# Kernel tuning notes

Hardware: AMD Instinct MI355X
Metric: run time of the kernel (lower is better)

Reference implementation:

```python
import jax, jax.numpy as jnp
import numpy as np

N_QUBITS = 10
N_LAYERS = 2
DIM = 2 ** N_QUBITS


def setup_inputs() -> dict:
    key = jax.random.key(0)
    kx, kw = jax.random.split(key)
    x = jax.random.normal(kx, (16384, DIM), dtype=jnp.float32)
    weights = jax.random.normal(kw, (N_LAYERS, N_QUBITS, 3), dtype=jnp.float32)
    return {"x": x, "weights": weights}


def _rot(phi, theta, omega):
    # qml.Rot(phi, theta, omega) = RZ(omega) @ RY(theta) @ RZ(phi)
    c = jnp.cos(theta / 2).astype(jnp.complex64)
    s = jnp.sin(theta / 2).astype(jnp.complex64)
    ep = jnp.exp(0.5j * phi.astype(jnp.complex64))
    eo = jnp.exp(0.5j * omega.astype(jnp.complex64))
    return jnp.stack([
        jnp.stack([jnp.conj(eo) * jnp.conj(ep) * c, -jnp.conj(eo) * ep * s]),
        jnp.stack([eo * jnp.conj(ep) * s, eo * ep * c]),
    ])


def _apply_1q(state, U, w):
    # state: [B, 2, 2, ..., 2]; wire w lives at axis w+1 (wire 0 = most significant)
    state = jnp.moveaxis(state, w + 1, 1)
    state = jnp.einsum('ij,bj...->bi...', U, state)
    return jnp.moveaxis(state, 1, w + 1)


def _cnot(state, c, t):
    state = jnp.moveaxis(state, (c + 1, t + 1), (1, 2))
    state = state.at[:, 1].set(state[:, 1, ::-1])  # flip target where control==1
    return jnp.moveaxis(state, (1, 2), (c + 1, t + 1))


def _pauliz_signs():
    # S[k, i] = +1 if bit i of basis index k is 0 else -1 (wire 0 most significant)
    idx = np.arange(DIM)
    S = np.stack([1.0 - 2.0 * ((idx >> (N_QUBITS - 1 - i)) & 1)
                  for i in range(N_QUBITS)], axis=1)
    return jnp.asarray(S.astype(np.float32))


def reference(x, weights):
    B = x.shape[0]
    x = x.reshape(B, -1)
    # AmplitudeEmbedding(normalize=True)
    amp = x / jnp.linalg.norm(x, axis=1, keepdims=True)
    state = amp.astype(jnp.complex64).reshape((B,) + (2,) * N_QUBITS)
    # StronglyEntanglingLayers: per layer, Rot on every wire then ring of CNOTs
    for l in range(N_LAYERS):
        for q in range(N_QUBITS):
            phi, theta, omega = weights[l, q, 0], weights[l, q, 1], weights[l, q, 2]
            state = _apply_1q(state, _rot(phi, theta, omega), q)
        r = (l % (N_QUBITS - 1)) + 1  # PennyLane default ranges
        for q in range(N_QUBITS):
            state = _cnot(state, q, (q + r) % N_QUBITS)
    probs = (state.real ** 2 + state.imag ** 2).reshape(B, DIM)
    return probs @ _pauliz_signs()  # [B, n_qubits] PauliZ expvals
```

## Files before the change

kernel.cpp:

```cpp
#include <hip/hip_runtime.h>
#include <math.h>

#define NQ 10
#define DIM 1024
#define NL 2

__global__ void precompute_gates(const float* __restrict__ w, float* __restrict__ g) {
    int t = threadIdx.x;
    if (t < NL * NQ) {
        float phi = w[t * 3 + 0], theta = w[t * 3 + 1], omega = w[t * 3 + 2];
        float c  = cosf(0.5f * theta), s = sinf(0.5f * theta);
        float ap = 0.5f * phi, ao = 0.5f * omega;
        float cs = cosf(ap + ao), ss = sinf(ap + ao);
        float cd = cosf(ap - ao), sd = sinf(ap - ao);
        float* o = g + t * 8;
        o[0] =  c * cs;  o[1] = -c * ss;
        o[2] = -s * cd;  o[3] = -s * sd;
        o[4] =  s * cd;  o[5] = -s * sd;
        o[6] =  c * cs;  o[7] =  c * ss;
    }
}

template<int CTRL>
__device__ __forceinline__ float dppmov(float v) {
    return __int_as_float(
        __builtin_amdgcn_mov_dpp(__float_as_int(v), CTRL, 0xF, 0xF, true));
}

typedef unsigned u32x2 __attribute__((ext_vector_type(2)));
typedef float f2 __attribute__((ext_vector_type(2)));

template<int LM>
__device__ __forceinline__ void plswap(float& d, float& s) {
#if __has_builtin(__builtin_amdgcn_permlane16_swap) && __has_builtin(__builtin_amdgcn_permlane32_swap)
    u32x2 r;
    if constexpr (LM == 16)
        r = __builtin_amdgcn_permlane16_swap(__float_as_uint(d), __float_as_uint(s), false, false);
    else
        r = __builtin_amdgcn_permlane32_swap(__float_as_uint(d), __float_as_uint(s), false, false);
    d = __uint_as_float(r.x);
    s = __uint_as_float(r.y);
#else
    asm("v_mov_b32 %0, %1" : "=v"(s) : "v"(s));
    if constexpr (LM == 16) asm("v_permlane16_swap_b32 %0, %1" : "+v"(d), "+v"(s));
    else                    asm("v_permlane32_swap_b32 %0, %1" : "+v"(d), "+v"(s));
#endif
}

template<int LM>
__device__ __forceinline__ float xfetch(float v) {
    if constexpr (LM == 1)      return dppmov<0xB1>(v);
    else if constexpr (LM == 2) return dppmov<0x4E>(v);
    else if constexpr (LM == 4)
        return __int_as_float(__builtin_amdgcn_ds_swizzle(__float_as_int(v), 0x101F));
    else                        return dppmov<0x128>(v);
}

template<int LM>
__device__ __forceinline__ f2 xfetch2(f2 v) {
    f2 r; r.x = xfetch<LM>(v.x); r.y = xfetch<LM>(v.y); return r;
}

template<int LM>
__device__ __forceinline__ void plswap2(f2 v, f2& d, f2& s) {
    float dx = v.x, sx = v.x; plswap<LM>(dx, sx);
    float dy = v.y, sy = v.y; plswap<LM>(dy, sy);
    d.x = dx; d.y = dy; s.x = sx; s.y = sy;
}

template<int LM>
__device__ __forceinline__ float bfly_add(float v) {
    if constexpr (LM >= 16) { float d = v, s = v; plswap<LM>(d, s); return d + s; }
    else                    return v + xfetch<LM>(v);
}

__device__ __forceinline__ float bfly_full(float v) {
    v = bfly_add<1>(v); v = bfly_add<2>(v); v = bfly_add<4>(v);
    v = bfly_add<8>(v); v = bfly_add<16>(v); v = bfly_add<32>(v);
    return v;
}

template<int P>
__device__ __forceinline__ void rot2(f2 (&R)[8], f2 (&I)[8],
                                     const float* __restrict__ g, int lane) {
    float u00r = g[0], u00i = g[1], u01r = g[2], u01i = g[3];
    float u10r = g[4], u10i = g[5], u11r = g[6], u11i = g[7];
    if constexpr (P == 0) {
        f2 Kr0 = {u00r, u10r}, Ki0 = {u00i, u10i};
        f2 Kr1 = {u01r, u11r}, Ki1 = {u01i, u11i};
        #pragma unroll
        for (int j = 0; j < 8; ++j) {
            f2 ar = R[j], ai = I[j];
            f2 arx = {ar.x, ar.x}, ary = {ar.y, ar.y};
            f2 aix = {ai.x, ai.x}, aiy = {ai.y, ai.y};
            R[j] = Kr0*arx - Ki0*aix + Kr1*ary - Ki1*aiy;
            I[j] = Kr0*aix + Ki0*arx + Kr1*aiy + Ki1*ary;
        }
    } else if constexpr (P <= 3) {
        constexpr int m2 = 1 << (P - 1);
        #pragma unroll
        for (int j = 0; j < 8; ++j) {
            if (!(j & m2)) {
                const int j2 = j | m2;
                f2 a0 = R[j], a0i = I[j], a1 = R[j2], a1i = I[j2];
                R[j]  = u00r*a0 - u00i*a0i + u01r*a1 - u01i*a1i;
                I[j]  = u00r*a0i + u00i*a0 + u01r*a1i + u01i*a1;
                R[j2] = u10r*a0 - u10i*a0i + u11r*a1 - u11i*a1i;
                I[j2] = u10r*a0i + u10i*a0 + u11r*a1i + u11i*a1;
            }
        }
    } else if constexpr (P <= 7) {
        constexpr int LM = 1 << (P - 4);
        const bool hi = (lane & LM) != 0;
        float Ar = hi ? u11r : u00r, Ai = hi ? u11i : u00i;
        float Br = hi ? u10r : u01r, Bi = hi ? u10i : u01i;
        #pragma unroll
        for (int j = 0; j < 8; ++j) {
            f2 pr = xfetch2<LM>(R[j]), pi = xfetch2<LM>(I[j]);
            f2 mr = R[j], mi = I[j];
            R[j] = Ar*mr - Ai*mi + Br*pr - Bi*pi;
            I[j] = Ar*mi + Ai*mr + Br*pi + Bi*pr;
        }
    } else {
        constexpr int LM = 1 << (P - 4);
        const bool hi = (lane & LM) != 0;
        float Cdr = hi ? u10r : u00r, Cdi = hi ? u10i : u00i;
        float Csr = hi ? u11r : u01r, Csi = hi ? u11i : u01i;
        #pragma unroll
        for (int j = 0; j < 8; ++j) {
            f2 dr, sr, di, si;
            plswap2<LM>(R[j], dr, sr);
            plswap2<LM>(I[j], di, si);
            R[j] = Cdr*dr - Cdi*di + Csr*sr - Csi*si;
            I[j] = Cdr*di + Cdi*dr + Csr*si + Csi*sr;
        }
    }
}

template<int PC, int PT>
__device__ __forceinline__ void cnot2(f2 (&R)[8], f2 (&I)[8], int lane) {
    if constexpr (PC >= 4 && PT >= 4) {
        constexpr int LM = 1 << (PT - 4);
        const bool ctrl = (lane & (1 << (PC - 4))) != 0;
        if constexpr (LM >= 16) {
            const bool t = (lane & LM) != 0;
            const bool sel = (ctrl == t);
            #pragma unroll
            for (int j = 0; j < 8; ++j) {
                f2 d, s;  plswap2<LM>(R[j], d, s);  R[j] = sel ? d : s;
                f2 di, si; plswap2<LM>(I[j], di, si); I[j] = sel ? di : si;
            }
        } else {
            #pragma unroll
            for (int j = 0; j < 8; ++j) {
                f2 pr = xfetch2<LM>(R[j]), pi = xfetch2<LM>(I[j]);
                R[j] = ctrl ? pr : R[j];
                I[j] = ctrl ? pi : I[j];
            }
        }
    } else if constexpr (PC >= 4 && PT >= 1) {
        constexpr int m2 = 1 << (PT - 1);
        const bool ctrl = (lane & (1 << (PC - 4))) != 0;
        #pragma unroll
        for (int j = 0; j < 8; ++j) {
            if (!(j & m2)) {
                const int j2 = j | m2;
                f2 a = R[j], b = R[j2];
                R[j] = ctrl ? b : a;  R[j2] = ctrl ? a : b;
                f2 c = I[j], d = I[j2];
                I[j] = ctrl ? d : c;  I[j2] = ctrl ? c : d;
            }
        }
    } else if constexpr (PC >= 4 && PT == 0) {
        const bool ctrl = (lane & (1 << (PC - 4))) != 0;
        #pragma unroll
        for (int j = 0; j < 8; ++j) {
            f2 a = R[j]; f2 sw; sw.x = a.y; sw.y = a.x; R[j] = ctrl ? sw : a;
            f2 b = I[j]; f2 sx; sx.x = b.y; sx.y = b.x; I[j] = ctrl ? sx : b;
        }
    } else if constexpr (PC >= 1 && PT >= 4) {
        constexpr int LM = 1 << (PT - 4);
        constexpr int cm2 = 1 << (PC - 1);
        if constexpr (LM >= 16) {
            const bool t = (lane & LM) != 0;
            #pragma unroll
            for (int j = 0; j < 8; ++j) {
                if (j & cm2) {
                    f2 d, s;  plswap2<LM>(R[j], d, s);  R[j] = t ? d : s;
                    f2 di, si; plswap2<LM>(I[j], di, si); I[j] = t ? di : si;
                }
            }
        } else {
            #pragma unroll
            for (int j = 0; j < 8; ++j) {
                if (j & cm2) { R[j] = xfetch2<LM>(R[j]); I[j] = xfetch2<LM>(I[j]); }
            }
        }
    } else if constexpr (PC == 0 && PT >= 4) {
        constexpr int LM = 1 << (PT - 4);
        if constexpr (LM >= 16) {
            const bool t = (lane & LM) != 0;
            #pragma unroll
            for (int j = 0; j < 8; ++j) {
                float dy = R[j].y, sy = R[j].y; plswap<LM>(dy, sy); R[j].y = t ? dy : sy;
                float ey = I[j].y, fy = I[j].y; plswap<LM>(ey, fy); I[j].y = t ? ey : fy;
            }
        } else {
            #pragma unroll
            for (int j = 0; j < 8; ++j) {
                R[j].y = xfetch<LM>(R[j].y); I[j].y = xfetch<LM>(I[j].y);
            }
        }
    } else if constexpr (PC >= 1 && PT >= 1) {
        constexpr int cm2 = 1 << (PC - 1), tm2 = 1 << (PT - 1);
        #pragma unroll
        for (int j = 0; j < 8; ++j) {
            if ((j & cm2) && !(j & tm2)) {
                const int j2 = j | tm2;
                f2 t = R[j]; R[j] = R[j2]; R[j2] = t;
                f2 u = I[j]; I[j] = I[j2]; I[j2] = u;
            }
        }
    } else if constexpr (PC >= 1 && PT == 0) {
        constexpr int cm2 = 1 << (PC - 1);
        #pragma unroll
        for (int j = 0; j < 8; ++j) {
            if (j & cm2) {
                f2 a = R[j]; R[j].x = a.y; R[j].y = a.x;
                f2 b = I[j]; I[j].x = b.y; I[j].y = b.x;
            }
        }
    } else {
        constexpr int tm2 = 1 << (PT - 1);
        #pragma unroll
        for (int j = 0; j < 8; ++j) {
            if (!(j & tm2)) {
                const int j2 = j | tm2;
                float t = R[j].y; R[j].y = R[j2].y; R[j2].y = t;
                float u = I[j].y; I[j].y = I[j2].y; I[j2].y = u;
            }
        }
    }
}

__global__ __launch_bounds__(256) void qsim(const float* __restrict__ x,
                                            const float* __restrict__ gates,
                                            float* __restrict__ out, int B) {
    const int lane = threadIdx.x & 63;
    const int wave = threadIdx.x >> 6;
    const int row  = blockIdx.x * 4 + wave;
    if (row >= B) return;

    const float* xr = x + (size_t)row * DIM + lane * 16;
    f2 R[8], I[8];
    {
        float4 v0 = *(const float4*)(xr + 0);
        float4 v1 = *(const float4*)(xr + 4);
        float4 v2 = *(const float4*)(xr + 8);
        float4 v3 = *(const float4*)(xr + 12);
        R[0].x=v0.x; R[0].y=v0.y;  R[1].x=v0.z; R[1].y=v0.w;
        R[2].x=v1.x; R[2].y=v1.y;  R[3].x=v1.z; R[3].y=v1.w;
        R[4].x=v2.x; R[4].y=v2.y;  R[5].x=v2.z; R[5].y=v2.w;
        R[6].x=v3.x; R[6].y=v3.y;  R[7].x=v3.z; R[7].y=v3.w;
    }
    f2 n2 = R[0]*R[0];
    #pragma unroll
    for (int j = 1; j < 8; ++j) n2 += R[j]*R[j];
    float nrm = bfly_full(n2.x + n2.y);
    float inv = rsqrtf(nrm);

    {
        const float* g = gates;
        const bool hi = (lane & 32) != 0;
        float Cdr = (hi ? g[4] : g[0]) * inv, Cdi = (hi ? g[5] : g[1]) * inv;
        float Csr = (hi ? g[6] : g[2]) * inv, Csi = (hi ? g[7] : g[3]) * inv;
        #pragma unroll
        for (int j = 0; j < 8; ++j) {
            f2 d, s; plswap2<32>(R[j], d, s);
            R[j] = Cdr*d + Csr*s;
            I[j] = Cdi*d + Csi*s;
        }
    }

    #define ROT(l, q) rot2<9 - (q)>(R, I, gates + ((l) * 10 + (q)) * 8, lane)

    ROT(0,1); ROT(0,2); ROT(0,3); ROT(0,4);
    ROT(0,5); ROT(0,6); ROT(0,7); ROT(0,8); ROT(0,9);
    cnot2<9,8>(R,I,lane); cnot2<8,7>(R,I,lane);
    cnot2<7,6>(R,I,lane); cnot2<6,5>(R,I,lane);
    cnot2<5,4>(R,I,lane); cnot2<4,3>(R,I,lane);
    cnot2<3,2>(R,I,lane); cnot2<2,1>(R,I,lane);
    cnot2<1,0>(R,I,lane); cnot2<0,9>(R,I,lane);

    ROT(1,0); ROT(1,1); ROT(1,2); ROT(1,3); ROT(1,4);
    ROT(1,5); ROT(1,6); ROT(1,7); ROT(1,8); ROT(1,9);
    cnot2<9,7>(R,I,lane); cnot2<8,6>(R,I,lane);
    cnot2<7,5>(R,I,lane); cnot2<6,4>(R,I,lane);
    cnot2<5,3>(R,I,lane); cnot2<4,2>(R,I,lane);
    cnot2<3,1>(R,I,lane); cnot2<2,0>(R,I,lane);
    cnot2<1,9>(R,I,lane); cnot2<0,8>(R,I,lane);

    #undef ROT

    f2 sum2 = {0.f, 0.f}, sa2 = {0.f, 0.f}, sb2 = {0.f, 0.f}, sc2 = {0.f, 0.f};
    #pragma unroll
    for (int j = 0; j < 8; ++j) {
        f2 t2 = R[j]*R[j] + I[j]*I[j];
        sum2 += t2;
        if (j & 4) sa2 += t2;
        if (j & 2) sb2 += t2;
        if (j & 1) sc2 += t2;
    }
    float sum = sum2.x + sum2.y;
    float s1a = sa2.x + sa2.y;
    float s1b = sb2.x + sb2.y;
    float s1c = sc2.x + sc2.y;
    float s1d = sum2.y;

    float w = sum;
    {
        float p, sg;
        sg = (lane & 1) ? -1.f : 1.f;  p = xfetch<1>(w); w = fmaf(sg, w, p);
        sg = (lane & 2) ? -1.f : 1.f;  p = xfetch<2>(w); w = fmaf(sg, w, p);
        sg = (lane & 4) ? -1.f : 1.f;  p = xfetch<4>(w); w = fmaf(sg, w, p);
        sg = (lane & 8) ? -1.f : 1.f;  p = xfetch<8>(w); w = fmaf(sg, w, p);
        { float d = w, s = w; plswap<16>(d, s); sg = (lane & 16) ? -1.f : 1.f; w = fmaf(sg, s, d); }
        { float d = w, s = w; plswap<32>(d, s); sg = (lane & 32) ? -1.f : 1.f; w = fmaf(sg, s, d); }
    }

    float R0 = bfly_full(s1a);
    float R1 = bfly_full(s1b);
    float R2 = bfly_full(s1c);
    float R3 = bfly_full(s1d);

    float* o = out + (size_t)row * NQ;
    if (lane && lane <= 32 && !(lane & (lane - 1)))
        o[6 - __ffs(lane)] = w;
    if (lane == 0) {
        o[6] = fmaf(-2.f, R0, w);
        o[7] = fmaf(-2.f, R1, w);
        o[8] = fmaf(-2.f, R2, w);
        o[9] = fmaf(-2.f, R3, w);
    }
}

extern "C" void kernel_launch(void* const* d_in, const int* in_sizes, int n_in,
                              void* d_out, int out_size, void* d_ws, size_t ws_size,
                              hipStream_t stream) {
    const float* x = (const float*)d_in[0];
    const float* w = (const float*)d_in[1];
    float* gates = (float*)d_ws;
    float* out = (float*)d_out;

    const int B = in_sizes[0] / DIM;

    precompute_gates<<<1, 64, 0, stream>>>(w, gates);
    qsim<<<(B + 3) / 4, 256, 0, stream>>>(x, gates, out, B);
}
```

Baseline: 170.4 us.

## Fold layer-1 CNOT ring into layer-2 rotations and parity-based readout

Removes the explicit CNOT ring after layer 0. Its permutation is folded into the layer-1 single-qubit gates, which become generalized gates whose partner index and coefficient selection depend on lane and register parities. The layer-1 CNOTs are likewise absorbed into the final PauliZ readout, computed as Walsh-Hadamard transforms over parity-signed accumulators with outputs picked from specific lanes. This saves the data-movement passes for 20 CNOTs but uses more cross-lane swizzle fetches (including ds_swizzle) and seven WHT reductions instead of four butterflies.

```diff
diff --git a/kernel.cpp b/kernel.cpp
--- a/kernel.cpp
+++ b/kernel.cpp
@@ -29,6 +29,8 @@
 
 typedef unsigned u32x2 __attribute__((ext_vector_type(2)));
 typedef float f2 __attribute__((ext_vector_type(2)));
+
+__device__ __forceinline__ f2 mk2(float a, float b) { f2 r; r.x = a; r.y = b; return r; }
 
 template<int LM>
 __device__ __forceinline__ void plswap(float& d, float& s) {
@@ -80,19 +82,49 @@
     return v;
 }
 
+template<int LM>
+__device__ __forceinline__ float lanefetch(float v, int lane) {
+    if constexpr (LM == 0)       return v;
+    else if constexpr (LM == 1)  return dppmov<0xB1>(v);
+    else if constexpr (LM == 2)  return dppmov<0x4E>(v);
+    else if constexpr (LM == 3)  return dppmov<0x1B>(v);
+    else if constexpr (LM == 6)
+        return __int_as_float(__builtin_amdgcn_ds_swizzle(__float_as_int(v), 0x181F));
+    else if constexpr (LM == 12)
+        return __int_as_float(__builtin_amdgcn_ds_swizzle(__float_as_int(v), 0x301F));
+    else if constexpr (LM == 24)
+        return __int_as_float(__builtin_amdgcn_ds_swizzle(__float_as_int(v), 0x601F));
+    else {
+        float t = __int_as_float(__builtin_amdgcn_ds_swizzle(__float_as_int(v), 0x401F));
+        float d = t, s = t; plswap<32>(d, s);
+        return (lane & 32) ? d : s;
+    }
+}
+
+__device__ __forceinline__ float wht64(float w, int lane) {
+    float p, sg;
+    sg = (lane & 1) ? -1.f : 1.f;  p = xfetch<1>(w); w = fmaf(sg, w, p);
+    sg = (lane & 2) ? -1.f : 1.f;  p = xfetch<2>(w); w = fmaf(sg, w, p);
+    sg = (lane & 4) ? -1.f : 1.f;  p = xfetch<4>(w); w = fmaf(sg, w, p);
+    sg = (lane & 8) ? -1.f : 1.f;  p = xfetch<8>(w); w = fmaf(sg, w, p);
+    { float d = w, s = w; plswap<16>(d, s); sg = (lane & 16) ? -1.f : 1.f; w = fmaf(sg, s, d); }
+    { float d = w, s = w; plswap<32>(d, s); sg = (lane & 32) ? -1.f : 1.f; w = fmaf(sg, s, d); }
+    return w;
+}
+
 template<int P>
 __device__ __forceinline__ void rot2(f2 (&R)[8], f2 (&I)[8],
                                      const float* __restrict__ g, int lane) {
     float u00r = g[0], u00i = g[1], u01r = g[2], u01i = g[3];
     float u10r = g[4], u10i = g[5], u11r = g[6], u11i = g[7];
     if constexpr (P == 0) {
-        f2 Kr0 = {u00r, u10r}, Ki0 = {u00i, u10i};
-        f2 Kr1 = {u01r, u11r}, Ki1 = {u01i, u11i};
+        f2 Kr0 = mk2(u00r, u10r), Ki0 = mk2(u00i, u10i);
+        f2 Kr1 = mk2(u01r, u11r), Ki1 = mk2(u01i, u11i);
         #pragma unroll
         for (int j = 0; j < 8; ++j) {
             f2 ar = R[j], ai = I[j];
-            f2 arx = {ar.x, ar.x}, ary = {ar.y, ar.y};
-            f2 aix = {ai.x, ai.x}, aiy = {ai.y, ai.y};
+            f2 arx = mk2(ar.x, ar.x), ary = mk2(ar.y, ar.y);
+            f2 aix = mk2(ai.x, ai.x), aiy = mk2(ai.y, ai.y);
             R[j] = Kr0*arx - Ki0*aix + Kr1*ary - Ki1*aiy;
             I[j] = Kr0*aix + Ki0*arx + Kr1*aiy + Ki1*ary;
         }
@@ -137,107 +169,75 @@
     }
 }
 
-template<int PC, int PT>
-__device__ __forceinline__ void cnot2(f2 (&R)[8], f2 (&I)[8], int lane) {
-    if constexpr (PC >= 4 && PT >= 4) {
-        constexpr int LM = 1 << (PT - 4);
-        const bool ctrl = (lane & (1 << (PC - 4))) != 0;
-        if constexpr (LM >= 16) {
-            const bool t = (lane & LM) != 0;
-            const bool sel = (ctrl == t);
-            #pragma unroll
-            for (int j = 0; j < 8; ++j) {
-                f2 d, s;  plswap2<LM>(R[j], d, s);  R[j] = sel ? d : s;
-                f2 di, si; plswap2<LM>(I[j], di, si); I[j] = sel ? di : si;
+template<int LMASK, int JMASK, int EB, int FL, int FJ, int FE>
+__device__ __forceinline__ void gate1(f2 (&R)[8], f2 (&I)[8],
+                                      const float* __restrict__ g, int lane) {
+    float u00r = g[0], u00i = g[1], u01r = g[2], u01i = g[3];
+    float u10r = g[4], u10i = g[5], u11r = g[6], u11i = g[7];
+    const bool lp = (__popc(lane & FL) & 1) != 0;
+    float ArL = lp ? u11r : u00r, ArH = lp ? u00r : u11r;
+    float AiL = lp ? u11i : u00i, AiH = lp ? u00i : u11i;
+    float BrL = lp ? u10r : u01r, BrH = lp ? u01r : u10r;
+    float BiL = lp ? u10i : u01i, BiH = lp ? u01i : u10i;
+    f2 cAr0, cAi0, cBr0, cBi0, cAr1, cAi1, cBr1, cBi1;
+    if constexpr (FE) {
+        cAr0 = mk2(ArL, ArH); cAi0 = mk2(AiL, AiH);
+        cBr0 = mk2(BrL, BrH); cBi0 = mk2(BiL, BiH);
+        cAr1 = mk2(ArH, ArL); cAi1 = mk2(AiH, AiL);
+        cBr1 = mk2(BrH, BrL); cBi1 = mk2(BiH, BiL);
+    } else {
+        cAr0 = mk2(ArL, ArL); cAi0 = mk2(AiL, AiL);
+        cBr0 = mk2(BrL, BrL); cBi0 = mk2(BiL, BiL);
+        cAr1 = mk2(ArH, ArH); cAi1 = mk2(AiH, AiH);
+        cBr1 = mk2(BrH, BrH); cBi1 = mk2(BiH, BiH);
+    }
+
+    if constexpr (JMASK == 0) {
+        #pragma unroll
+        for (int j = 0; j < 8; ++j) {
+            const int jp = __builtin_popcount(j & FJ) & 1;
+            f2 mr = R[j], mi = I[j];
+            f2 pr, pi;
+            if constexpr (EB) {
+                pr.x = lanefetch<LMASK>(mr.y, lane); pr.y = lanefetch<LMASK>(mr.x, lane);
+                pi.x = lanefetch<LMASK>(mi.y, lane); pi.y = lanefetch<LMASK>(mi.x, lane);
+            } else {
+                pr.x = lanefetch<LMASK>(mr.x, lane); pr.y = lanefetch<LMASK>(mr.y, lane);
+                pi.x = lanefetch<LMASK>(mi.x, lane); pi.y = lanefetch<LMASK>(mi.y, lane);
             }
-        } else {
-            #pragma unroll
-            for (int j = 0; j < 8; ++j) {
-                f2 pr = xfetch2<LM>(R[j]), pi = xfetch2<LM>(I[j]);
-                R[j] = ctrl ? pr : R[j];
-                I[j] = ctrl ? pi : I[j];
-            }
-        }
-    } else if constexpr (PC >= 4 && PT >= 1) {
-        constexpr int m2 = 1 << (PT - 1);
-        const bool ctrl = (lane & (1 << (PC - 4))) != 0;
-        #pragma unroll
-        for (int j = 0; j < 8; ++j) {
-            if (!(j & m2)) {
-                const int j2 = j | m2;
-                f2 a = R[j], b = R[j2];
-                R[j] = ctrl ? b : a;  R[j2] = ctrl ? a : b;
-                f2 c = I[j], d = I[j2];
-                I[j] = ctrl ? d : c;  I[j2] = ctrl ? c : d;
-            }
-        }
-    } else if constexpr (PC >= 4 && PT == 0) {
-        const bool ctrl = (lane & (1 << (PC - 4))) != 0;
-        #pragma unroll
-        for (int j = 0; j < 8; ++j) {
-            f2 a = R[j]; f2 sw; sw.x = a.y; sw.y = a.x; R[j] = ctrl ? sw : a;
-            f2 b = I[j]; f2 sx; sx.x = b.y; sx.y = b.x; I[j] = ctrl ? sx : b;
-        }
-    } else if constexpr (PC >= 1 && PT >= 4) {
-        constexpr int LM = 1 << (PT - 4);
-        constexpr int cm2 = 1 << (PC - 1);
-        if constexpr (LM >= 16) {
-            const bool t = (lane & LM) != 0;
-            #pragma unroll
-            for (int j = 0; j < 8; ++j) {
-                if (j & cm2) {
-                    f2 d, s;  plswap2<LM>(R[j], d, s);  R[j] = t ? d : s;
-                    f2 di, si; plswap2<LM>(I[j], di, si); I[j] = t ? di : si;
+            f2 Ar = jp ? cAr1 : cAr0, Ai = jp ? cAi1 : cAi0;
+            f2 Br = jp ? cBr1 : cBr0, Bi = jp ? cBi1 : cBi0;
+            R[j] = Ar*mr - Ai*mi + Br*pr - Bi*pi;
+            I[j] = Ar*mi + Ai*mr + Br*pi + Bi*pr;
+        }
+    } else {
+        #pragma unroll
+        for (int j = 0; j < 8; ++j) {
+            const int j2 = j ^ JMASK;
+            if (j < j2) {
+                f2 aR = R[j], aI = I[j], bR = R[j2], bI = I[j2];
+                f2 paR, paI, pbR, pbI;
+                if constexpr (EB) {
+                    paR.x = lanefetch<LMASK>(bR.y, lane); paR.y = lanefetch<LMASK>(bR.x, lane);
+                    paI.x = lanefetch<LMASK>(bI.y, lane); paI.y = lanefetch<LMASK>(bI.x, lane);
+                    pbR.x = lanefetch<LMASK>(aR.y, lane); pbR.y = lanefetch<LMASK>(aR.x, lane);
+                    pbI.x = lanefetch<LMASK>(aI.y, lane); pbI.y = lanefetch<LMASK>(aI.x, lane);
+                } else {
+                    paR.x = lanefetch<LMASK>(bR.x, lane); paR.y = lanefetch<LMASK>(bR.y, lane);
+                    paI.x = lanefetch<LMASK>(bI.x, lane); paI.y = lanefetch<LMASK>(bI.y, lane);
+                    pbR.x = lanefetch<LMASK>(aR.x, lane); pbR.y = lanefetch<LMASK>(aR.y, lane);
+                    pbI.x = lanefetch<LMASK>(aI.x, lane); pbI.y = lanefetch<LMASK>(aI.y, lane);
                 }
-            }
-        } else {
-            #pragma unroll
-            for (int j = 0; j < 8; ++j) {
-                if (j & cm2) { R[j] = xfetch2<LM>(R[j]); I[j] = xfetch2<LM>(I[j]); }
-            }
-        }
-    } else if constexpr (PC == 0 && PT >= 4) {
-        constexpr int LM = 1 << (PT - 4);
-        if constexpr (LM >= 16) {
-            const bool t = (lane & LM) != 0;
-            #pragma unroll
-            for (int j = 0; j < 8; ++j) {
-                float dy = R[j].y, sy = R[j].y; plswap<LM>(dy, sy); R[j].y = t ? dy : sy;
-                float ey = I[j].y, fy = I[j].y; plswap<LM>(ey, fy); I[j].y = t ? ey : fy;
-            }
-        } else {
-            #pragma unroll
-            for (int j = 0; j < 8; ++j) {
-                R[j].y = xfetch<LM>(R[j].y); I[j].y = xfetch<LM>(I[j].y);
-            }
-        }
-    } else if constexpr (PC >= 1 && PT >= 1) {
-        constexpr int cm2 = 1 << (PC - 1), tm2 = 1 << (PT - 1);
-        #pragma unroll
-        for (int j = 0; j < 8; ++j) {
-            if ((j & cm2) && !(j & tm2)) {
-                const int j2 = j | tm2;
-                f2 t = R[j]; R[j] = R[j2]; R[j2] = t;
-                f2 u = I[j]; I[j] = I[j2]; I[j2] = u;
-            }
-        }
-    } else if constexpr (PC >= 1 && PT == 0) {
-        constexpr int cm2 = 1 << (PC - 1);
-        #pragma unroll
-        for (int j = 0; j < 8; ++j) {
-            if (j & cm2) {
-                f2 a = R[j]; R[j].x = a.y; R[j].y = a.x;
-                f2 b = I[j]; I[j].x = b.y; I[j].y = b.x;
-            }
-        }
-    } else {
-        constexpr int tm2 = 1 << (PT - 1);
-        #pragma unroll
-        for (int j = 0; j < 8; ++j) {
-            if (!(j & tm2)) {
-                const int j2 = j | tm2;
-                float t = R[j].y; R[j].y = R[j2].y; R[j2].y = t;
-                float u = I[j].y; I[j].y = I[j2].y; I[j2].y = u;
+                const int jpa = __builtin_popcount(j  & FJ) & 1;
+                const int jpb = __builtin_popcount(j2 & FJ) & 1;
+                f2 Ara = jpa ? cAr1 : cAr0, Aia = jpa ? cAi1 : cAi0;
+                f2 Bra = jpa ? cBr1 : cBr0, Bia = jpa ? cBi1 : cBi0;
+                f2 Arb = jpb ? cAr1 : cAr0, Aib = jpb ? cAi1 : cAi0;
+                f2 Brb = jpb ? cBr1 : cBr0, Bib = jpb ? cBi1 : cBi0;
+                R[j]  = Ara*aR - Aia*aI + Bra*paR - Bia*paI;
+                I[j]  = Ara*aI + Aia*aR + Bra*paI + Bia*paR;
+                R[j2] = Arb*bR - Aib*bI + Brb*pbR - Bib*pbI;
+                I[j2] = Arb*bI + Aib*bR + Brb*pbI + Bib*pbR;
             }
         }
     }
@@ -258,16 +258,15 @@
         float4 v1 = *(const float4*)(xr + 4);
         float4 v2 = *(const float4*)(xr + 8);
         float4 v3 = *(const float4*)(xr + 12);
-        R[0].x=v0.x; R[0].y=v0.y;  R[1].x=v0.z; R[1].y=v0.w;
-        R[2].x=v1.x; R[2].y=v1.y;  R[3].x=v1.z; R[3].y=v1.w;
-        R[4].x=v2.x; R[4].y=v2.y;  R[5].x=v2.z; R[5].y=v2.w;
-        R[6].x=v3.x; R[6].y=v3.y;  R[7].x=v3.z; R[7].y=v3.w;
+        R[0] = mk2(v0.x, v0.y); R[1] = mk2(v0.z, v0.w);
+        R[2] = mk2(v1.x, v1.y); R[3] = mk2(v1.z, v1.w);
+        R[4] = mk2(v2.x, v2.y); R[5] = mk2(v2.z, v2.w);
+        R[6] = mk2(v3.x, v3.y); R[7] = mk2(v3.z, v3.w);
     }
     f2 n2 = R[0]*R[0];
     #pragma unroll
     for (int j = 1; j < 8; ++j) n2 += R[j]*R[j];
-    float nrm = bfly_full(n2.x + n2.y);
-    float inv = rsqrtf(nrm);
+    float inv = rsqrtf(bfly_full(n2.x + n2.y));
 
     {
         const float* g = gates;
@@ -282,66 +281,50 @@
         }
     }
 
-    #define ROT(l, q) rot2<9 - (q)>(R, I, gates + ((l) * 10 + (q)) * 8, lane)
-
-    ROT(0,1); ROT(0,2); ROT(0,3); ROT(0,4);
-    ROT(0,5); ROT(0,6); ROT(0,7); ROT(0,8); ROT(0,9);
-    cnot2<9,8>(R,I,lane); cnot2<8,7>(R,I,lane);
-    cnot2<7,6>(R,I,lane); cnot2<6,5>(R,I,lane);
-    cnot2<5,4>(R,I,lane); cnot2<4,3>(R,I,lane);
-    cnot2<3,2>(R,I,lane); cnot2<2,1>(R,I,lane);
-    cnot2<1,0>(R,I,lane); cnot2<0,9>(R,I,lane);
-
-    ROT(1,0); ROT(1,1); ROT(1,2); ROT(1,3); ROT(1,4);
-    ROT(1,5); ROT(1,6); ROT(1,7); ROT(1,8); ROT(1,9);
-    cnot2<9,7>(R,I,lane); cnot2<8,6>(R,I,lane);
-    cnot2<7,5>(R,I,lane); cnot2<6,4>(R,I,lane);
-    cnot2<5,3>(R,I,lane); cnot2<4,2>(R,I,lane);
-    cnot2<3,1>(R,I,lane); cnot2<2,0>(R,I,lane);
-    cnot2<1,9>(R,I,lane); cnot2<0,8>(R,I,lane);
-
-    #undef ROT
-
-    f2 sum2 = {0.f, 0.f}, sa2 = {0.f, 0.f}, sb2 = {0.f, 0.f}, sc2 = {0.f, 0.f};
+    #define ROT0(q) rot2<9 - (q)>(R, I, gates + (q) * 8, lane)
+    ROT0(1); ROT0(2); ROT0(3); ROT0(4);
+    ROT0(5); ROT0(6); ROT0(7); ROT0(8); ROT0(9);
+    #undef ROT0
+
+    const float* g1 = gates + 10 * 8;
+    gate1<48, 0, 0, 31, 7, 1>(R, I, g1 + 0*8, lane);
+    gate1<24, 0, 0, 48, 0, 0>(R, I, g1 + 1*8, lane);
+    gate1<12, 0, 0, 56, 0, 0>(R, I, g1 + 2*8, lane);
+    gate1< 6, 0, 0, 60, 0, 0>(R, I, g1 + 3*8, lane);
+    gate1< 3, 0, 0, 62, 0, 0>(R, I, g1 + 4*8, lane);
+    gate1< 1, 4, 0, 63, 0, 0>(R, I, g1 + 5*8, lane);
+    gate1< 0, 6, 0, 63, 4, 0>(R, I, g1 + 6*8, lane);
+    gate1< 0, 3, 0, 63, 6, 0>(R, I, g1 + 7*8, lane);
+    gate1< 0, 1, 1, 63, 7, 0>(R, I, g1 + 8*8, lane);
+    gate1<48, 0, 1, 63, 7, 1>(R, I, g1 + 9*8, lane);
+
+    f2 ac0 = mk2(0.f,0.f), ac1 = ac0, ac3 = ac0, ac4 = ac0, ac6 = ac0, ac7 = ac0;
     #pragma unroll
     for (int j = 0; j < 8; ++j) {
         f2 t2 = R[j]*R[j] + I[j]*I[j];
-        sum2 += t2;
-        if (j & 4) sa2 += t2;
-        if (j & 2) sb2 += t2;
-        if (j & 1) sc2 += t2;
-    }
-    float sum = sum2.x + sum2.y;
-    float s1a = sa2.x + sa2.y;
-    float s1b = sb2.x + sb2.y;
-    float s1c = sc2.x + sc2.y;
-    float s1d = sum2.y;
-
-    float w = sum;
-    {
-        float p, sg;
-        sg = (lane & 1) ? -1.f : 1.f;  p = xfetch<1>(w); w = fmaf(sg, w, p);
-        sg = (lane & 2) ? -1.f : 1.f;  p = xfetch<2>(w); w = fmaf(sg, w, p);
-        sg = (lane & 4) ? -1.f : 1.f;  p = xfetch<4>(w); w = fmaf(sg, w, p);
-        sg = (lane & 8) ? -1.f : 1.f;  p = xfetch<8>(w); w = fmaf(sg, w, p);
-        { float d = w, s = w; plswap<16>(d, s); sg = (lane & 16) ? -1.f : 1.f; w = fmaf(sg, s, d); }
-        { float d = w, s = w; plswap<32>(d, s); sg = (lane & 32) ? -1.f : 1.f; w = fmaf(sg, s, d); }
-    }
-
-    float R0 = bfly_full(s1a);
-    float R1 = bfly_full(s1b);
-    float R2 = bfly_full(s1c);
-    float R3 = bfly_full(s1d);
+        ac0 += t2;
+        if (__builtin_popcount(j & 1) & 1) ac1 -= t2; else ac1 += t2;
+        if (__builtin_popcount(j & 3) & 1) ac3 -= t2; else ac3 += t2;
+        if (__builtin_popcount(j & 4) & 1) ac4 -= t2; else ac4 += t2;
+        if (__builtin_popcount(j & 6) & 1) ac6 -= t2; else ac6 += t2;
+        if (__builtin_popcount(j & 7) & 1) ac7 -= t2; else ac7 += t2;
+    }
+    float W1 = wht64(ac3.x + ac3.y, lane);
+    float W2 = wht64(ac1.x - ac1.y, lane);
+    float W3 = wht64(ac7.x - ac7.y, lane);
+    float W4 = wht64(ac0.x + ac0.y, lane);
+    float W5 = wht64(ac3.x - ac3.y, lane);
+    float W6 = wht64(ac6.x + ac6.y, lane);
+    float W7 = wht64(ac4.x - ac4.y, lane);
 
     float* o = out + (size_t)row * NQ;
-    if (lane && lane <= 32 && !(lane & (lane - 1)))
-        o[6 - __ffs(lane)] = w;
-    if (lane == 0) {
-        o[6] = fmaf(-2.f, R0, w);
-        o[7] = fmaf(-2.f, R1, w);
-        o[8] = fmaf(-2.f, R2, w);
-        o[9] = fmaf(-2.f, R3, w);
-    }
+    if      (lane == 6)  { o[0] = W1; }
+    else if (lane == 3)  { o[1] = W2; }
+    else if (lane == 51) { o[9] = W2; o[5] = W4; }
+    else if (lane == 39) { o[2] = W3; }
+    else if (lane == 25) { o[4] = W3; o[8] = W7; }
+    else if (lane == 12) { o[3] = W4; o[7] = W6; }
+    else if (lane == 38) { o[6] = W5; }
 }
 
 extern "C" void kernel_launch(void* const* d_in, const int* in_sizes, int n_in,
```

After: 159.8 us. 6.2% less time.
